# Performance work log

Measured on AMD Instinct MI355X. Metric: run time of the kernel, lower is better.

Reference implementation:

```python
import jax, jax.numpy as jnp
import numpy as np

MAX_DISPARITY = 192
D = MAX_DISPARITY // 4  # 48 disparity levels


def setup_inputs() -> dict:
    key = jax.random.key(0)
    k1, k2 = jax.random.split(key)
    B, C, H, W = 4, 32, 64, 128
    left = jax.random.normal(k1, (B, C, H, W), dtype=jnp.float32)
    right = jax.random.normal(k2, (B, C, H, W), dtype=jnp.float32)
    return {"left": left, "right": right}


def reference(left, right):
    # left, right: [B, C, H, W] -> cost: [B, 2C, D, H, W]
    B, C, H, W = left.shape
    d = jnp.arange(D)[:, None]        # [D, 1]
    w = jnp.arange(W)[None, :]        # [1, W]
    mask = (w >= d).astype(left.dtype)  # [D, W]: valid columns for disparity d

    # left half: left[b,c,h,w] where w >= d, else 0
    left_vol = left[:, :, None, :, :] * mask[None, None, :, None, :]

    # right half: right[b,c,h,w-d] where w >= d, else 0 (clip keeps gather in-bounds;
    # out-of-range positions are zeroed by the mask)
    idx = jnp.clip(w - d, 0)                      # [D, W]
    right_shift = jnp.take(right, idx, axis=-1)   # [B, C, H, D, W]
    right_vol = jnp.transpose(right_shift, (0, 1, 3, 2, 4)) * mask[None, None, :, None, :]

    return jnp.concatenate([left_vol, right_vol], axis=1)  # [B, 2C, D, H, W]
```

## Files before the change

### kernel.cpp

```cpp
#include <hip/hip_runtime.h>

#define BB 4
#define CC 32
#define HH 64
#define WW 128
#define DD 48

__global__ __launch_bounds__(256) void cost_vol_kernel(
    const float* __restrict__ left,
    const float* __restrict__ right,
    float* __restrict__ out)
{
    __shared__ float lds_r[2][160];

    const int bx = blockIdx.x;
    const int hp = bx & 31;
    const int c  = (bx >> 5) & 31;
    const int b  = bx >> 10;
    const int h0 = hp << 1;

    const int t = threadIdx.x;

    {
        const int row = t >> 7;
        const int i   = t & 127;
        const float* rrow = right + (((b * CC + c) * HH) + h0 + row) * WW;
        lds_r[row][i + (i >> 2)] = rrow[i];
    }

    const int w4    = t & 31;
    const int h_loc = (t >> 5) & 1;
    const int dg    = t >> 6;
    const int w0    = w4 << 2;

    const float* lrow = left + (((b * CC + c) * HH) + h0 + h_loc) * WW;
    const float4 lv = *reinterpret_cast<const float4*>(lrow + w0);

    __syncthreads();

    const float* rl = lds_r[h_loc];

    const size_t baseL =
        ((((size_t)(b * 2 * CC + c) * DD + dg) * HH) + h0 + h_loc) * WW + w0;
    float* pL = out + baseL;
    float* pR = pL + (size_t)CC * DD * HH * WW;

    #pragma unroll
    for (int iter = 0; iter < 12; ++iter) {
        const int d = dg + (iter << 2);
        const int e = w0 - d;

        float4 vl, vr;
        {
            int i0 = e;     int x0 = i0 < 0 ? 0 : i0; float r0 = rl[x0 + (x0 >> 2)];
            int i1 = e + 1; int x1 = i1 < 0 ? 0 : i1; float r1 = rl[x1 + (x1 >> 2)];
            int i2 = e + 2; int x2 = i2 < 0 ? 0 : i2; float r2 = rl[x2 + (x2 >> 2)];
            int i3 = e + 3; int x3 = i3 < 0 ? 0 : i3; float r3 = rl[x3 + (x3 >> 2)];
            vl.x = (i0 >= 0) ? lv.x : 0.0f;  vr.x = (i0 >= 0) ? r0 : 0.0f;
            vl.y = (i1 >= 0) ? lv.y : 0.0f;  vr.y = (i1 >= 0) ? r1 : 0.0f;
            vl.z = (i2 >= 0) ? lv.z : 0.0f;  vr.z = (i2 >= 0) ? r2 : 0.0f;
            vl.w = (i3 >= 0) ? lv.w : 0.0f;  vr.w = (i3 >= 0) ? r3 : 0.0f;
        }
        *reinterpret_cast<float4*>(pL) = vl;
        *reinterpret_cast<float4*>(pR) = vr;

        pL += 4 * HH * WW;
        pR += 4 * HH * WW;
    }
}

extern "C" void kernel_launch(void* const* d_in, const int* in_sizes, int n_in,
                              void* d_out, int out_size, void* d_ws, size_t ws_size,
                              hipStream_t stream) {
    const float* left  = (const float*)d_in[0];
    const float* right = (const float*)d_in[1];
    float* out = (float*)d_out;

    const int grid  = BB * CC * (HH / 2);
    const int block = 256;
    cost_vol_kernel<<<grid, block, 0, stream>>>(left, right, out);
}
```

Measured before the change: 77.48 us.

## Enlarge per-block tile to 16 rows and use nontemporal vector stores

Each block now handles 16 image rows with 512 threads, and each thread loops over all 48 disparities instead of 12. Right-image rows are loaded into LDS with float4 loads. Output writes use nontemporal stores to avoid polluting caches on a pure streaming write. The grid shrinks eightfold, which reduces block launch overhead but may leave fewer waves in flight to hide store latency.

```diff
diff --git a/kernel.cpp b/kernel.cpp
--- a/kernel.cpp
+++ b/kernel.cpp
@@ -5,33 +5,39 @@
 #define HH 64
 #define WW 128
 #define DD 48
+#define HT 16
+#define RSTRIDE 160
 
-__global__ __launch_bounds__(256) void cost_vol_kernel(
+typedef float f32x4 __attribute__((ext_vector_type(4)));
+
+__global__ __launch_bounds__(512) void cost_vol_kernel(
     const float* __restrict__ left,
     const float* __restrict__ right,
     float* __restrict__ out)
 {
-    __shared__ float lds_r[2][160];
+    __shared__ float lds_r[HT][RSTRIDE];
 
     const int bx = blockIdx.x;
-    const int hp = bx & 31;
-    const int c  = (bx >> 5) & 31;
-    const int b  = bx >> 10;
-    const int h0 = hp << 1;
+    const int hq = bx & 3;
+    const int c  = (bx >> 2) & 31;
+    const int b  = bx >> 7;
+    const int h0 = hq * HT;
 
-    const int t = threadIdx.x;
+    const int t     = threadIdx.x;
+    const int w4    = t & 31;
+    const int h_loc = t >> 5;
+    const int w0    = w4 << 2;
 
     {
-        const int row = t >> 7;
-        const int i   = t & 127;
+        const int row = t >> 5;
+        const int i0  = (t & 31) << 2;
         const float* rrow = right + (((b * CC + c) * HH) + h0 + row) * WW;
-        lds_r[row][i + (i >> 2)] = rrow[i];
+        float4 rv = *reinterpret_cast<const float4*>(rrow + i0);
+        lds_r[row][(i0    ) + ((i0    ) >> 2)] = rv.x;
+        lds_r[row][(i0 + 1) + ((i0 + 1) >> 2)] = rv.y;
+        lds_r[row][(i0 + 2) + ((i0 + 2) >> 2)] = rv.z;
+        lds_r[row][(i0 + 3) + ((i0 + 3) >> 2)] = rv.w;
     }
-
-    const int w4    = t & 31;
-    const int h_loc = (t >> 5) & 1;
-    const int dg    = t >> 6;
-    const int w0    = w4 << 2;
 
     const float* lrow = left + (((b * CC + c) * HH) + h0 + h_loc) * WW;
     const float4 lv = *reinterpret_cast<const float4*>(lrow + w0);
@@ -40,32 +46,33 @@
 
     const float* rl = lds_r[h_loc];
 
-    const size_t baseL =
-        ((((size_t)(b * 2 * CC + c) * DD + dg) * HH) + h0 + h_loc) * WW + w0;
-    float* pL = out + baseL;
+    float* pL = out + ((((size_t)(b * 2 * CC + c) * DD) * HH) + h0 + h_loc) * WW + w0;
     float* pR = pL + (size_t)CC * DD * HH * WW;
 
-    #pragma unroll
-    for (int iter = 0; iter < 12; ++iter) {
-        const int d = dg + (iter << 2);
+    #pragma unroll 6
+    for (int d = 0; d < DD; ++d) {
         const int e = w0 - d;
 
-        float4 vl, vr;
-        {
-            int i0 = e;     int x0 = i0 < 0 ? 0 : i0; float r0 = rl[x0 + (x0 >> 2)];
-            int i1 = e + 1; int x1 = i1 < 0 ? 0 : i1; float r1 = rl[x1 + (x1 >> 2)];
-            int i2 = e + 2; int x2 = i2 < 0 ? 0 : i2; float r2 = rl[x2 + (x2 >> 2)];
-            int i3 = e + 3; int x3 = i3 < 0 ? 0 : i3; float r3 = rl[x3 + (x3 >> 2)];
-            vl.x = (i0 >= 0) ? lv.x : 0.0f;  vr.x = (i0 >= 0) ? r0 : 0.0f;
-            vl.y = (i1 >= 0) ? lv.y : 0.0f;  vr.y = (i1 >= 0) ? r1 : 0.0f;
-            vl.z = (i2 >= 0) ? lv.z : 0.0f;  vr.z = (i2 >= 0) ? r2 : 0.0f;
-            vl.w = (i3 >= 0) ? lv.w : 0.0f;  vr.w = (i3 >= 0) ? r3 : 0.0f;
-        }
-        *reinterpret_cast<float4*>(pL) = vl;
-        *reinterpret_cast<float4*>(pR) = vr;
+        const int i0 = e;     const int x0 = i0 < 0 ? 0 : i0;
+        const int i1 = e + 1; const int x1 = i1 < 0 ? 0 : i1;
+        const int i2 = e + 2; const int x2 = i2 < 0 ? 0 : i2;
+        const int i3 = e + 3; const int x3 = i3 < 0 ? 0 : i3;
+        const float r0 = rl[x0 + (x0 >> 2)];
+        const float r1 = rl[x1 + (x1 >> 2)];
+        const float r2 = rl[x2 + (x2 >> 2)];
+        const float r3 = rl[x3 + (x3 >> 2)];
 
-        pL += 4 * HH * WW;
-        pR += 4 * HH * WW;
+        f32x4 vl, vr;
+        vl.x = (i0 >= 0) ? lv.x : 0.0f;  vr.x = (i0 >= 0) ? r0 : 0.0f;
+        vl.y = (i1 >= 0) ? lv.y : 0.0f;  vr.y = (i1 >= 0) ? r1 : 0.0f;
+        vl.z = (i2 >= 0) ? lv.z : 0.0f;  vr.z = (i2 >= 0) ? r2 : 0.0f;
+        vl.w = (i3 >= 0) ? lv.w : 0.0f;  vr.w = (i3 >= 0) ? r3 : 0.0f;
+
+        __builtin_nontemporal_store(vl, reinterpret_cast<f32x4*>(pL));
+        __builtin_nontemporal_store(vr, reinterpret_cast<f32x4*>(pR));
+
+        pL += HH * WW;
+        pR += HH * WW;
     }
 }
 
@@ -76,7 +83,7 @@
     const float* right = (const float*)d_in[1];
     float* out = (float*)d_out;
 
-    const int grid  = BB * CC * (HH / 2);
-    const int block = 256;
+    const int grid  = BB * CC * (HH / HT);
+    const int block = 512;
     cost_vol_kernel<<<grid, block, 0, stream>>>(left, right, out);
 }
```

Measured after the change: 73.98 us. 1.05x faster.
